# Kernel tuning notes

Measured on AMD Instinct MI355X. Metric: run time of the kernel, lower is better.

The kernel has to match this reference:

```python
import jax, jax.numpy as jnp
import numpy as np

D_MODEL = 1024
D_INNER = 2048  # d_model * expand_factor
EPS = 1e-6


def setup_inputs() -> dict:
    key = jax.random.key(0)
    ks = jax.random.split(key, 9)
    s_in = 1.0 / np.sqrt(D_MODEL)
    s_out = 1.0 / np.sqrt(D_INNER)
    x = jax.random.normal(ks[0], (4, 2048, D_MODEL), dtype=jnp.float32)
    # weights stored as [in, out] (transpose of nn.Linear layout)
    Wq = jax.random.uniform(ks[1], (D_MODEL, D_INNER), jnp.float32, -s_in, s_in)
    bq = jax.random.uniform(ks[2], (D_INNER,), jnp.float32, -s_in, s_in)
    Wk = jax.random.uniform(ks[3], (D_MODEL, D_INNER), jnp.float32, -s_in, s_in)
    bk = jax.random.uniform(ks[4], (D_INNER,), jnp.float32, -s_in, s_in)
    Wv = jax.random.uniform(ks[5], (D_MODEL, D_INNER), jnp.float32, -s_in, s_in)
    bv = jax.random.uniform(ks[6], (D_INNER,), jnp.float32, -s_in, s_in)
    Wo = jax.random.uniform(ks[7], (D_INNER, D_MODEL), jnp.float32, -s_out, s_out)
    bo = jax.random.uniform(ks[8], (D_MODEL,), jnp.float32, -s_out, s_out)
    return {"x": x, "Wq": Wq, "bq": bq, "Wk": Wk, "bk": bk,
            "Wv": Wv, "bv": bv, "Wo": Wo, "bo": bo}


def _phi(x):
    """ELU + 1 feature map (positive features)."""
    return jax.nn.elu(x) + 1.0


def reference(x, Wq, bq, Wk, bk, Wv, bv, Wo, bo):
    # x: [B, N, d_model]
    Q = _phi(x @ Wq + bq)          # [B, N, d_inner]
    K = _phi(x @ Wk + bk)          # [B, N, d_inner]
    V = x @ Wv + bv                # [B, N, d_inner]
    n = x.shape[1]
    # Causal linear attention; identical math to cumsum-of-outer-products:
    # numerator_n = sum_{m<=n} (Q_n . K_m) V_m ; denominator_n = sum_{m<=n} Q_n . K_m
    scores = jnp.einsum("bnd,bmd->bnm", Q, K)            # [B, N, N]
    mask = jnp.tril(jnp.ones((n, n), dtype=scores.dtype))
    scores = scores * mask
    numerator = jnp.einsum("bnm,bme->bne", scores, V)    # [B, N, d_inner]
    denominator = scores.sum(axis=-1, keepdims=True) + EPS
    out = numerator / denominator
    return out @ Wo + bo           # [B, N, d_model] (dropout is identity in eval)
```

## Files before the change

kernel.cpp:

```cpp
#include <hip/hip_runtime.h>
#include <hip/hip_bf16.h>


#define D_MODEL 1024
#define D_INNER 2048
#define SEQ     2048
#define NBATCH  4
#define MTOT    (NBATCH * SEQ)

typedef __attribute__((ext_vector_type(8))) __bf16 bf16x8;
typedef __attribute__((ext_vector_type(4))) float  f32x4;
typedef __attribute__((ext_vector_type(8))) short  short8v;
typedef __attribute__((ext_vector_type(4))) int    int4v;
typedef __attribute__((ext_vector_type(8))) int    int8v;

__device__ __forceinline__ short f2bf(float f) {
  union { float f; unsigned u; } x; x.f = f;
  unsigned r = x.u + 0x7fffu + ((x.u >> 16) & 1u);
  return (short)(r >> 16);
}
__device__ __forceinline__ float bf2f(short s) {
  union { unsigned u; float f; } x; x.u = ((unsigned)(unsigned short)s) << 16;
  return x.f;
}

__device__ __forceinline__ unsigned char f2fp8(float f) {
  union { float f; unsigned u; } x; x.f = f;
  const unsigned s = (x.u >> 24) & 0x80u;
  const unsigned a = x.u & 0x7fffffffu;
  if (a >= 0x43E00000u) return (unsigned char)(s | 0x7Eu);
  if (a < 0x3C800000u) {
    union { float f; unsigned u; } y; y.u = a;
    const int mi = (int)rintf(y.f * 512.0f);
    return (unsigned char)(s | (unsigned)mi);
  }
  const unsigned r = a + 0x7FFFFu + ((a >> 20) & 1u);
  const unsigned E = (r >> 23) - 120u;
  return (unsigned char)(s | (E << 3) | ((r >> 20) & 7u));
}

typedef const void __attribute__((address_space(1)))* as1cv;
typedef void __attribute__((address_space(3)))* as3v;

__device__ __forceinline__ void gload_lds16(const void* g, void* l) {
  __builtin_amdgcn_global_load_lds((as1cv)g, (as3v)l, 16, 0, 0);
}

__device__ __forceinline__ f32x4 mfma16(bf16x8 a, bf16x8 b, f32x4 c) {
  return __builtin_amdgcn_mfma_f32_16x16x32_bf16(a, b, c, 0, 0, 0);
}

__device__ __forceinline__ f32x4 mfma_fp8(int8v a, int8v b, f32x4 c) {
  asm("v_mfma_f32_16x16x128_f8f6f4 %0, %1, %2, %0"
      : "+v"(c) : "v"(a), "v"(b));
  return c;
}

__device__ __forceinline__ void gemm_pipe(const short* __restrict__ A, int lda, int aRowBase,
                                          const short* __restrict__ B, int ldb, int bRowBase,
                                          int k0, int k1, short* smem, f32x4 acc[4][4]) {
  const int t    = threadIdx.x;
  const int lane = t & 63, wid = t >> 6;
  const int wr = wid >> 1, wc = wid & 1;
  const int lrow = lane & 15, kblk = lane >> 4;

  const int r0 = t >> 2;
  const int sc = ((t & 3) ^ ((t >> 3) & 3)) * 8;
  const short* pA = A + (size_t)(aRowBase + r0) * lda + (k0 + sc);
  const short* pB = B + (size_t)(bRowBase + r0) * ldb + (k0 + sc);
  const size_t rA = (size_t)64 * lda;
  const size_t rB = (size_t)64 * ldb;

  int aoff[4], boff[4];
#pragma unroll
  for (int m = 0; m < 4; ++m) {
    const int row = wr * 64 + m * 16 + lrow;
    aoff[m] = (row * 64 + kblk * 16) ^ (((row >> 1) & 3) << 4);
  }
#pragma unroll
  for (int n = 0; n < 4; ++n) {
    const int row = wc * 64 + n * 16 + lrow;
    boff[n] = (row * 64 + kblk * 16) ^ (((row >> 1) & 3) << 4);
  }
  const char* cs = (const char*)smem;

#define STG(bufShorts) do {                                                    \
    gload_lds16(pA, smem + (bufShorts) + t * 8);                               \
    gload_lds16(pA + rA, smem + (bufShorts) + 2048 + t * 8);                   \
    gload_lds16(pB, smem + (bufShorts) + 4096 + t * 8);                        \
    gload_lds16(pB + rB, smem + (bufShorts) + 6144 + t * 8);                   \
    pA += 32; pB += 32;                                                        \
  } while (0)

#define CSTEP(bufBytes) do {                                                   \
    bf16x8 a[4], b[4];                                                         \
    _Pragma("unroll") for (int m = 0; m < 4; ++m)                              \
      a[m] = *(const bf16x8*)(cs + (bufBytes) + aoff[m]);                      \
    _Pragma("unroll") for (int n = 0; n < 4; ++n)                              \
      b[n] = *(const bf16x8*)(cs + (bufBytes) + 8192 + boff[n]);               \
    _Pragma("unroll") for (int m = 0; m < 4; ++m)                              \
      _Pragma("unroll") for (int n = 0; n < 4; ++n)                            \
        acc[m][n] = mfma16(a[m], b[n], acc[m][n]);                             \
  } while (0)

  STG(0);
  __syncthreads();
  for (int k = k0; k < k1; k += 64) {
    if (k + 32 < k1) STG(8192);
    CSTEP(0);
    __syncthreads();
    if (k + 64 < k1) STG(0);
    CSTEP(16384);
    __syncthreads();
  }
#undef STG
#undef CSTEP
}

__device__ __forceinline__ void gemm_pipe8(const unsigned char* __restrict__ A, int lda, int aRowBase,
                                           const unsigned char* __restrict__ B, int ldb, int bRowBase,
                                           int k0, int k1, char* smem, f32x4 acc[4][4]) {
  const int t    = threadIdx.x;
  const int lane = t & 63, wid = t >> 6;
  const int wr = wid >> 1, wc = wid & 1;
  const int lrow = lane & 15, kblk = lane >> 4;

  const int srow = t >> 3;
  const int scol = (((t & 7) ^ ((t >> 3) & 7)) << 4);
  const unsigned char* pA = A + (size_t)(aRowBase + srow) * lda + (k0 + scol);
  const unsigned char* pB = B + (size_t)(bRowBase + srow) * ldb + (k0 + scol);

  int aoff[4][2], boff[4][2];
#pragma unroll
  for (int m = 0; m < 4; ++m) {
    const int row = wr * 64 + m * 16 + lrow;
#pragma unroll
    for (int j = 0; j < 2; ++j)
      aoff[m][j] = row * 128 + (((kblk * 2 + j) ^ (row & 7)) << 4);
  }
#pragma unroll
  for (int n = 0; n < 4; ++n) {
    const int row = wc * 64 + n * 16 + lrow;
#pragma unroll
    for (int j = 0; j < 2; ++j)
      boff[n][j] = row * 128 + (((kblk * 2 + j) ^ (row & 7)) << 4);
  }

#define STG8(bufB) do {                                                        \
    _Pragma("unroll") for (int i = 0; i < 4; ++i) {                            \
      gload_lds16(pA + (size_t)(32 * i) * lda, smem + (bufB) + i * 4096 + t * 16);      \
      gload_lds16(pB + (size_t)(32 * i) * ldb, smem + (bufB) + 16384 + i * 4096 + t * 16); \
    }                                                                          \
    pA += 128; pB += 128;                                                      \
  } while (0)

#define CSTEP8(bufB) do {                                                      \
    int8v a[4], b[4];                                                          \
    _Pragma("unroll") for (int m = 0; m < 4; ++m)                              \
      _Pragma("unroll") for (int j = 0; j < 2; ++j)                            \
        ((int4v*)&a[m])[j] = *(const int4v*)(smem + (bufB) + aoff[m][j]);      \
    _Pragma("unroll") for (int n = 0; n < 4; ++n)                              \
      _Pragma("unroll") for (int j = 0; j < 2; ++j)                            \
        ((int4v*)&b[n])[j] = *(const int4v*)(smem + (bufB) + 16384 + boff[n][j]); \
    _Pragma("unroll") for (int m = 0; m < 4; ++m)                              \
      _Pragma("unroll") for (int n = 0; n < 4; ++n)                            \
        acc[m][n] = mfma_fp8(a[m], b[n], acc[m][n]);                           \
  } while (0)

  STG8(0);
  __syncthreads();
  for (int k = k0; k < k1; k += 256) {
    if (k + 128 < k1) STG8(32768);
    CSTEP8(0);
    __syncthreads();
    if (k + 256 < k1) STG8(0);
    CSTEP8(32768);
    __syncthreads();
  }
#undef STG8
#undef CSTEP8
}

#define GEMM_PRE                                           \
  __shared__ __align__(16) short smem[4 * 4096];           \
  f32x4 acc[4][4];                                         \
  _Pragma("unroll")                                        \
  for (int m = 0; m < 4; ++m)                              \
    _Pragma("unroll")                                      \
    for (int n = 0; n < 4; ++n) acc[m][n] = (f32x4){0.f, 0.f, 0.f, 0.f};

#define GEMM_PRE8                                          \
  __shared__ __align__(16) char smem8[65536];              \
  f32x4 acc[4][4];                                         \
  _Pragma("unroll")                                        \
  for (int m = 0; m < 4; ++m)                              \
    _Pragma("unroll")                                      \
    for (int n = 0; n < 4; ++n) acc[m][n] = (f32x4){0.f, 0.f, 0.f, 0.f};

#define EPILOG_VARS                                        \
  const int lane = threadIdx.x & 63;                       \
  const int wid  = threadIdx.x >> 6;                       \
  const int wr = wid >> 1, wc = wid & 1;                   \
  const int lrow = lane & 15, kblk = lane >> 4;

__device__ __forceinline__ void retile_store(const short* smem, short* dst0, int ldd) {
  const int er  = threadIdx.x >> 1;
  const int hf  = threadIdx.x & 1;
  short* dst = dst0 + (size_t)er * ldd + hf * 64;
#pragma unroll
  for (int i = 0; i < 8; ++i) {
    int byte = er * 256 + hf * 128 + i * 16;
    byte ^= (er & 7) << 5;
    ((short8v*)dst)[i] = *(const short8v*)((const char*)smem + byte);
  }
}

__global__ __launch_bounds__(256) void k_proj_qk8(const unsigned char* __restrict__ X8,
                                                  const unsigned char* __restrict__ WT8,
                                                  const float* __restrict__ bq,
                                                  const float* __restrict__ bk,
                                                  unsigned char* __restrict__ Qm8,
                                                  unsigned char* __restrict__ Km8) {
  GEMM_PRE8
  const int blockM = blockIdx.y * 128;
  const int blockN = blockIdx.x * 128;
  gemm_pipe8(X8, D_MODEL, blockM, WT8, D_MODEL, blockN, 0, D_MODEL, smem8, acc);
  EPILOG_VARS
  const int seg = blockN >> 11;
  const float* bias = (seg == 0) ? bq : bk;
  unsigned char* dst = (seg == 0) ? Qm8 : Km8;
#pragma unroll
  for (int m = 0; m < 4; ++m)
#pragma unroll
    for (int n = 0; n < 4; ++n) {
      const int e = (blockN & 2047) + wc * 64 + n * 16 + lrow;
      const float bvv = bias[e];
#pragma unroll
      for (int j = 0; j < 4; ++j) {
        const int row = blockM + wr * 64 + m * 16 + kblk * 4 + j;
        float v = acc[m][n][j] + bvv;
        v = (v > 0.f) ? (v + 1.f) : __expf(v);
        dst[(size_t)row * D_INNER + e] = f2fp8(v);
      }
    }
}

__global__ __launch_bounds__(256) void k_wfuse(const short* __restrict__ WvB,
                                               const short* __restrict__ WoT,
                                               short* __restrict__ wfT) {
  GEMM_PRE
  const int blockM = blockIdx.y * 128;
  const int blockN = blockIdx.x * 128;
  gemm_pipe(WvB, D_INNER, blockM, WoT, D_INNER, blockN, 0, D_INNER, smem, acc);
  EPILOG_VARS
#pragma unroll
  for (int m = 0; m < 4; ++m)
#pragma unroll
    for (int n = 0; n < 4; ++n) {
      const int cl = wc * 64 + n * 16 + lrow;
#pragma unroll
      for (int j = 0; j < 4; ++j) {
        const int rl = wr * 64 + m * 16 + kblk * 4 + j;
        int byte = cl * 256 + rl * 2;
        byte ^= (cl & 7) << 5;
        *(short*)((char*)smem + byte) = f2bf(acc[m][n][j]);
      }
    }
  __syncthreads();
  retile_store(smem, wfT + (size_t)blockN * D_MODEL + blockM, D_MODEL);
}

__global__ __launch_bounds__(256) void k_bfuse(const float* __restrict__ bv,
                                               const float* __restrict__ Wo,
                                               float* __restrict__ bfuse) {
  const int o = blockIdx.x;
  const int t = threadIdx.x;
  float s = 0.f;
#pragma unroll
  for (int e = t; e < D_INNER; e += 256)
    s += bv[e] * Wo[(size_t)e * D_MODEL + o];
#pragma unroll
  for (int off = 32; off >= 1; off >>= 1) s += __shfl_down(s, off, 64);
  __shared__ float ws[4];
  if ((t & 63) == 0) ws[t >> 6] = s;
  __syncthreads();
  if (t == 0) bfuse[o] = ws[0] + ws[1] + ws[2] + ws[3];
}

__global__ __launch_bounds__(256) void k_w2(const short* __restrict__ X,
                                            const short* __restrict__ WfT,
                                            const float* __restrict__ bfuse,
                                            short* __restrict__ w2T) {
  GEMM_PRE
  const int blockM = blockIdx.y * 128;
  const int blockN = blockIdx.x * 128;
  gemm_pipe(X, D_MODEL, blockM, WfT, D_MODEL, blockN, 0, D_MODEL, smem, acc);
  EPILOG_VARS
#pragma unroll
  for (int m = 0; m < 4; ++m)
#pragma unroll
    for (int n = 0; n < 4; ++n) {
      const int cl = wc * 64 + n * 16 + lrow;
      const float bvv = bfuse[blockN + cl];
#pragma unroll
      for (int j = 0; j < 4; ++j) {
        const int rl = wr * 64 + m * 16 + kblk * 4 + j;
        int byte = cl * 256 + rl * 2;
        byte ^= (cl & 7) << 5;
        *(short*)((char*)smem + byte) = f2bf(acc[m][n][j] + bvv);
      }
    }
  __syncthreads();
  const int b   = blockM >> 11;
  const int mm0 = blockM & 2047;
  retile_store(smem, w2T + ((size_t)b * D_MODEL + blockN) * SEQ + mm0, SEQ);
}

__global__ __launch_bounds__(256) void k_qkt8(const unsigned char* __restrict__ Q8,
                                              const unsigned char* __restrict__ K8,
                                              short* __restrict__ S,
                                              float* __restrict__ den_part) {
  const int b = blockIdx.y;
  const int t = blockIdx.x;
  int ib = (int)((-1.0f + sqrtf(8.0f * (float)t + 1.0f)) * 0.5f);
  while ((ib + 1) * (ib + 2) / 2 <= t) ++ib;
  while (ib * (ib + 1) / 2 > t) --ib;
  const int jb = t - ib * (ib + 1) / 2;
  GEMM_PRE8
  short* Sb = S + (size_t)b * SEQ * SEQ;
  gemm_pipe8(Q8 + (size_t)b * SEQ * D_INNER, D_INNER, ib * 128,
             K8 + (size_t)b * SEQ * D_INNER, D_INNER, jb * 128,
             0, D_INNER, smem8, acc);
  EPILOG_VARS
  const bool diag = (jb == ib);
  float sums[4][4];
#pragma unroll
  for (int m = 0; m < 4; ++m)
#pragma unroll
    for (int j = 0; j < 4; ++j) sums[m][j] = 0.f;
#pragma unroll
  for (int m = 0; m < 4; ++m)
#pragma unroll
    for (int n = 0; n < 4; ++n) {
      const int col = jb * 128 + wc * 64 + n * 16 + lrow;
#pragma unroll
      for (int j = 0; j < 4; ++j) {
        const int row = ib * 128 + wr * 64 + m * 16 + kblk * 4 + j;
        float v = acc[m][n][j];
        if (diag && col > row) v = 0.f;
        const short bs = f2bf(v);
        Sb[(size_t)row * SEQ + col] = bs;
        sums[m][j] += bf2f(bs);
      }
    }
#pragma unroll
  for (int m = 0; m < 4; ++m)
#pragma unroll
    for (int j = 0; j < 4; ++j) {
      float red = sums[m][j];
      red += __shfl_xor(red, 1, 64);
      red += __shfl_xor(red, 2, 64);
      red += __shfl_xor(red, 4, 64);
      red += __shfl_xor(red, 8, 64);
      if (lrow == 0) {
        const int rloc = wr * 64 + m * 16 + kblk * 4 + j;
        den_part[(size_t)(2 * jb + wc) * MTOT + b * SEQ + ib * 128 + rloc] = red;
      }
    }
}

__global__ __launch_bounds__(256) void k_sv(const short* __restrict__ S,
                                            const short* __restrict__ W2T,
                                            const float* __restrict__ den_part,
                                            const float* __restrict__ bo,
                                            float* __restrict__ out) {
  const int b = blockIdx.z;
  const int ib = 15 - blockIdx.y;
  const int eb = blockIdx.x;
  __shared__ float dnm[128];
  {
    const int t = threadIdx.x;
    if (t < 128) {
      float s = 1e-6f;
      const int nv = 2 * (ib + 1);
      const float* dp = den_part + b * SEQ + ib * 128 + t;
      for (int q = 0; q < nv; ++q) s += dp[(size_t)q * MTOT];
      dnm[t] = 1.0f / s;
    }
  }
  GEMM_PRE
  gemm_pipe(S + (size_t)b * SEQ * SEQ, SEQ, ib * 128,
            W2T + (size_t)b * (size_t)D_MODEL * SEQ, SEQ, eb * 128,
            0, (ib + 1) * 128, smem, acc);
  EPILOG_VARS
  const int blockM = ib * 128;
#pragma unroll
  for (int m = 0; m < 4; ++m)
#pragma unroll
    for (int j = 0; j < 4; ++j) {
      const int rloc = wr * 64 + m * 16 + kblk * 4 + j;
      const int row = blockM + rloc;
      const float rcp = dnm[rloc];
#pragma unroll
      for (int n = 0; n < 4; ++n) {
        const int col = eb * 128 + wc * 64 + n * 16 + lrow;
        out[((size_t)(b * SEQ + row)) * D_MODEL + col] = acc[m][n][j] * rcp + bo[col];
      }
    }
}

__global__ void k_cvt(const float* __restrict__ in, short* __restrict__ outb,
                      unsigned char* __restrict__ out8, int n4) {
  int i = blockIdx.x * blockDim.x + threadIdx.x;
  const int stride = gridDim.x * blockDim.x;
  for (; i < n4; i += stride) {
    float4 v = ((const float4*)in)[i];
    short4 o;
    o.x = f2bf(v.x); o.y = f2bf(v.y); o.z = f2bf(v.z); o.w = f2bf(v.w);
    ((short4*)outb)[i] = o;
    uchar4 q;
    q.x = f2fp8(v.x); q.y = f2fp8(v.y); q.z = f2fp8(v.z); q.w = f2fp8(v.w);
    ((uchar4*)out8)[i] = q;
  }
}

__global__ __launch_bounds__(256) void k_transposeAll(const float* __restrict__ w0,
                                                      const float* __restrict__ w1,
                                                      const float* __restrict__ w2,
                                                      const float* __restrict__ w3,
                                                      unsigned char* __restrict__ wqkT8,
                                                      short* __restrict__ wvB,
                                                      short* __restrict__ woT) {
  __shared__ float tl[32][33];
  const int z = blockIdx.z;
  const float* in = (z == 0) ? w0 : (z == 1) ? w1 : (z == 2) ? w2 : w3;
  const int R = (z < 3) ? 1024 : 2048;
  const int C = (z < 3) ? 2048 : 1024;
  const int nbx = C >> 5;
  const int c0 = (blockIdx.x % nbx) * 32, r0 = (blockIdx.x / nbx) * 32;
  const int tx = threadIdx.x & 31, ty = (threadIdx.x >> 5) * 4;
  if (z == 2) {
#pragma unroll
    for (int i = 0; i < 4; ++i) {
      const size_t idx = (size_t)(r0 + ty + i) * C + (c0 + tx);
      wvB[idx] = f2bf(in[idx]);
    }
    return;
  }
#pragma unroll
  for (int i = 0; i < 4; ++i)
    tl[ty + i][tx] = in[(size_t)(r0 + ty + i) * C + (c0 + tx)];
  __syncthreads();
  if (z < 2) {
    unsigned char* o = wqkT8 + (size_t)z * D_INNER * D_MODEL;
#pragma unroll
    for (int i = 0; i < 4; ++i)
      o[(size_t)(c0 + ty + i) * R + (r0 + tx)] = f2fp8(tl[tx][ty + i]);
  } else {
#pragma unroll
    for (int i = 0; i < 4; ++i)
      woT[(size_t)(c0 + ty + i) * R + (r0 + tx)] = f2bf(tl[tx][ty + i]);
  }
}

extern "C" void kernel_launch(void* const* d_in, const int* in_sizes, int n_in,
                              void* d_out, int out_size, void* d_ws, size_t ws_size,
                              hipStream_t stream) {
  const float* x  = (const float*)d_in[0];
  const float* Wq = (const float*)d_in[1];
  const float* bq = (const float*)d_in[2];
  const float* Wk = (const float*)d_in[3];
  const float* bk = (const float*)d_in[4];
  const float* Wv = (const float*)d_in[5];
  const float* bv = (const float*)d_in[6];
  const float* Wo = (const float*)d_in[7];
  const float* bo = (const float*)d_in[8];
  float* out = (float*)d_out;

  short* xb    = (short*)d_ws;
  short* wvB   = xb    + (size_t)MTOT * D_MODEL;
  short* woT   = wvB   + (size_t)D_MODEL * D_INNER;
  short* wfT   = woT   + (size_t)D_MODEL * D_INNER;
  short* Sc    = wfT   + (size_t)D_MODEL * D_MODEL;
  short* w2T   = Sc    + (size_t)NBATCH * SEQ * SEQ;
  unsigned char* x8    = (unsigned char*)(w2T + (size_t)NBATCH * D_MODEL * SEQ);
  unsigned char* wqkT8 = x8    + (size_t)MTOT * D_MODEL;
  unsigned char* Qm8   = wqkT8 + (size_t)2 * D_INNER * D_MODEL;
  unsigned char* Km8   = Qm8   + (size_t)MTOT * D_INNER;
  float* den_part      = (float*)(Km8 + (size_t)MTOT * D_INNER);
  float* bfuse         = den_part + (size_t)32 * MTOT;

  dim3 b256(256);
  k_cvt<<<2048, b256, 0, stream>>>(x, xb, x8, MTOT * D_MODEL / 4);
  k_transposeAll<<<dim3(2048, 1, 4), b256, 0, stream>>>(Wq, Wk, Wv, Wo, wqkT8, wvB, woT);

  k_bfuse<<<1024, b256, 0, stream>>>(bv, Wo, bfuse);
  k_wfuse<<<dim3(8, 8), b256, 0, stream>>>(wvB, woT, wfT);

  k_proj_qk8<<<dim3(32, 64), b256, 0, stream>>>(x8, wqkT8, bq, bk, Qm8, Km8);
  k_qkt8<<<dim3(136, NBATCH), b256, 0, stream>>>(Qm8, Km8, Sc, den_part);

  k_w2<<<dim3(8, 64), b256, 0, stream>>>(xb, wfT, bfuse, w2T);
  k_sv<<<dim3(8, 16, NBATCH), b256, 0, stream>>>(Sc, w2T, den_part, bo, out);
}
```

Baseline: 263.6 us.

## Merge preprocessing kernels and use single-buffered fp8 QK^T pipeline

Three preprocessing kernels (x conversion, weight transpose/cast, fused bias) are combined into one launch that dispatches by block index, removing two kernel launches and their gaps. Separately, the QK^T fp8 GEMM switches to a single-buffered 32KB LDS loop with one K-step of 128 per iteration. The smaller LDS footprint may allow more blocks per CU, but it gives up overlapping loads with MFMA compute. In the merged kernel, a block that returns early in the Wv path is harmless, since that path has no barrier after the return.

Result: no change. 262.4 us (median of 2 runs) (-0.4%).

```diff
diff --git a/kernel.cpp b/kernel.cpp
--- a/kernel.cpp
+++ b/kernel.cpp
@@ -181,6 +181,63 @@
 #undef CSTEP8
 }
 
+__device__ __forceinline__ void gemm_pipe8s(const unsigned char* __restrict__ A, int lda, int aRowBase,
+                                            const unsigned char* __restrict__ B, int ldb, int bRowBase,
+                                            int k0, int k1, char* smem, f32x4 acc[4][4]) {
+  const int t    = threadIdx.x;
+  const int lane = t & 63, wid = t >> 6;
+  const int wr = wid >> 1, wc = wid & 1;
+  const int lrow = lane & 15, kblk = lane >> 4;
+
+  const int srow = t >> 3;
+  const int scol = (((t & 7) ^ ((t >> 3) & 7)) << 4);
+  const unsigned char* pA = A + (size_t)(aRowBase + srow) * lda + (k0 + scol);
+  const unsigned char* pB = B + (size_t)(bRowBase + srow) * ldb + (k0 + scol);
+
+  int aoff[4][2], boff[4][2];
+#pragma unroll
+  for (int m = 0; m < 4; ++m) {
+    const int row = wr * 64 + m * 16 + lrow;
+#pragma unroll
+    for (int j = 0; j < 2; ++j)
+      aoff[m][j] = row * 128 + (((kblk * 2 + j) ^ (row & 7)) << 4);
+  }
+#pragma unroll
+  for (int n = 0; n < 4; ++n) {
+    const int row = wc * 64 + n * 16 + lrow;
+#pragma unroll
+    for (int j = 0; j < 2; ++j)
+      boff[n][j] = row * 128 + (((kblk * 2 + j) ^ (row & 7)) << 4);
+  }
+
+  for (int k = k0; k < k1; k += 128) {
+#pragma unroll
+    for (int i = 0; i < 4; ++i) {
+      gload_lds16(pA + (size_t)(32 * i) * lda, smem + i * 4096 + t * 16);
+      gload_lds16(pB + (size_t)(32 * i) * ldb, smem + 16384 + i * 4096 + t * 16);
+    }
+    pA += 128; pB += 128;
+    __syncthreads();
+    int8v a[4], b[4];
+#pragma unroll
+    for (int m = 0; m < 4; ++m)
+#pragma unroll
+      for (int j = 0; j < 2; ++j)
+        ((int4v*)&a[m])[j] = *(const int4v*)(smem + aoff[m][j]);
+#pragma unroll
+    for (int n = 0; n < 4; ++n)
+#pragma unroll
+      for (int j = 0; j < 2; ++j)
+        ((int4v*)&b[n])[j] = *(const int4v*)(smem + 16384 + boff[n][j]);
+#pragma unroll
+    for (int m = 0; m < 4; ++m)
+#pragma unroll
+      for (int n = 0; n < 4; ++n)
+        acc[m][n] = mfma_fp8(a[m], b[n], acc[m][n]);
+    __syncthreads();
+  }
+}
+
 #define GEMM_PRE                                           \
   __shared__ __align__(16) short smem[4 * 4096];           \
   f32x4 acc[4][4];                                         \
@@ -191,6 +248,14 @@
 
 #define GEMM_PRE8                                          \
   __shared__ __align__(16) char smem8[65536];              \
+  f32x4 acc[4][4];                                         \
+  _Pragma("unroll")                                        \
+  for (int m = 0; m < 4; ++m)                              \
+    _Pragma("unroll")                                      \
+    for (int n = 0; n < 4; ++n) acc[m][n] = (f32x4){0.f, 0.f, 0.f, 0.f};
+
+#define GEMM_PRE8S                                         \
+  __shared__ __align__(16) char smem8[32768];              \
   f32x4 acc[4][4];                                         \
   _Pragma("unroll")                                        \
   for (int m = 0; m < 4; ++m)                              \
@@ -270,23 +335,6 @@
   retile_store(smem, wfT + (size_t)blockN * D_MODEL + blockM, D_MODEL);
 }
 
-__global__ __launch_bounds__(256) void k_bfuse(const float* __restrict__ bv,
-                                               const float* __restrict__ Wo,
-                                               float* __restrict__ bfuse) {
-  const int o = blockIdx.x;
-  const int t = threadIdx.x;
-  float s = 0.f;
-#pragma unroll
-  for (int e = t; e < D_INNER; e += 256)
-    s += bv[e] * Wo[(size_t)e * D_MODEL + o];
-#pragma unroll
-  for (int off = 32; off >= 1; off >>= 1) s += __shfl_down(s, off, 64);
-  __shared__ float ws[4];
-  if ((t & 63) == 0) ws[t >> 6] = s;
-  __syncthreads();
-  if (t == 0) bfuse[o] = ws[0] + ws[1] + ws[2] + ws[3];
-}
-
 __global__ __launch_bounds__(256) void k_w2(const short* __restrict__ X,
                                             const short* __restrict__ WfT,
                                             const float* __restrict__ bfuse,
@@ -326,11 +374,11 @@
   while ((ib + 1) * (ib + 2) / 2 <= t) ++ib;
   while (ib * (ib + 1) / 2 > t) --ib;
   const int jb = t - ib * (ib + 1) / 2;
-  GEMM_PRE8
+  GEMM_PRE8S
   short* Sb = S + (size_t)b * SEQ * SEQ;
-  gemm_pipe8(Q8 + (size_t)b * SEQ * D_INNER, D_INNER, ib * 128,
-             K8 + (size_t)b * SEQ * D_INNER, D_INNER, jb * 128,
-             0, D_INNER, smem8, acc);
+  gemm_pipe8s(Q8 + (size_t)b * SEQ * D_INNER, D_INNER, ib * 128,
+              K8 + (size_t)b * SEQ * D_INNER, D_INNER, jb * 128,
+              0, D_INNER, smem8, acc);
   EPILOG_VARS
   const bool diag = (jb == ib);
   float sums[4][4];
@@ -409,57 +457,77 @@
     }
 }
 
-__global__ void k_cvt(const float* __restrict__ in, short* __restrict__ outb,
-                      unsigned char* __restrict__ out8, int n4) {
-  int i = blockIdx.x * blockDim.x + threadIdx.x;
-  const int stride = gridDim.x * blockDim.x;
-  for (; i < n4; i += stride) {
-    float4 v = ((const float4*)in)[i];
-    short4 o;
-    o.x = f2bf(v.x); o.y = f2bf(v.y); o.z = f2bf(v.z); o.w = f2bf(v.w);
-    ((short4*)outb)[i] = o;
-    uchar4 q;
-    q.x = f2fp8(v.x); q.y = f2fp8(v.y); q.z = f2fp8(v.z); q.w = f2fp8(v.w);
-    ((uchar4*)out8)[i] = q;
-  }
-}
-
-__global__ __launch_bounds__(256) void k_transposeAll(const float* __restrict__ w0,
-                                                      const float* __restrict__ w1,
-                                                      const float* __restrict__ w2,
-                                                      const float* __restrict__ w3,
-                                                      unsigned char* __restrict__ wqkT8,
-                                                      short* __restrict__ wvB,
-                                                      short* __restrict__ woT) {
+__global__ __launch_bounds__(256) void k_pre(const float* __restrict__ x,
+                                             const float* __restrict__ Wq,
+                                             const float* __restrict__ Wk,
+                                             const float* __restrict__ Wv,
+                                             const float* __restrict__ Wo,
+                                             const float* __restrict__ bv,
+                                             short* __restrict__ xb,
+                                             unsigned char* __restrict__ x8,
+                                             unsigned char* __restrict__ wqkT8,
+                                             short* __restrict__ wvB,
+                                             short* __restrict__ woT,
+                                             float* __restrict__ bfuse) {
   __shared__ float tl[32][33];
-  const int z = blockIdx.z;
-  const float* in = (z == 0) ? w0 : (z == 1) ? w1 : (z == 2) ? w2 : w3;
-  const int R = (z < 3) ? 1024 : 2048;
-  const int C = (z < 3) ? 2048 : 1024;
-  const int nbx = C >> 5;
-  const int c0 = (blockIdx.x % nbx) * 32, r0 = (blockIdx.x / nbx) * 32;
-  const int tx = threadIdx.x & 31, ty = (threadIdx.x >> 5) * 4;
-  if (z == 2) {
-#pragma unroll
-    for (int i = 0; i < 4; ++i) {
-      const size_t idx = (size_t)(r0 + ty + i) * C + (c0 + tx);
-      wvB[idx] = f2bf(in[idx]);
-    }
-    return;
-  }
-#pragma unroll
-  for (int i = 0; i < 4; ++i)
-    tl[ty + i][tx] = in[(size_t)(r0 + ty + i) * C + (c0 + tx)];
-  __syncthreads();
-  if (z < 2) {
-    unsigned char* o = wqkT8 + (size_t)z * D_INNER * D_MODEL;
+  __shared__ float ws[4];
+  const int bid = blockIdx.x;
+  if (bid < 2048) {
+    const int n4 = MTOT * D_MODEL / 4;
+    int i = bid * 256 + threadIdx.x;
+    const int stride = 2048 * 256;
+    for (; i < n4; i += stride) {
+      float4 v = ((const float4*)x)[i];
+      short4 o;
+      o.x = f2bf(v.x); o.y = f2bf(v.y); o.z = f2bf(v.z); o.w = f2bf(v.w);
+      ((short4*)xb)[i] = o;
+      uchar4 q;
+      q.x = f2fp8(v.x); q.y = f2fp8(v.y); q.z = f2fp8(v.z); q.w = f2fp8(v.w);
+      ((uchar4*)x8)[i] = q;
+    }
+  } else if (bid < 2048 + 4 * 2048) {
+    const int z  = (bid - 2048) >> 11;
+    const int bx = (bid - 2048) & 2047;
+    const float* in = (z == 0) ? Wq : (z == 1) ? Wk : (z == 2) ? Wv : Wo;
+    const int R = (z < 3) ? 1024 : 2048;
+    const int C = (z < 3) ? 2048 : 1024;
+    const int nbx = C >> 5;
+    const int c0 = (bx % nbx) * 32, r0 = (bx / nbx) * 32;
+    const int tx = threadIdx.x & 31, ty = (threadIdx.x >> 5) * 4;
+    if (z == 2) {
+#pragma unroll
+      for (int i = 0; i < 4; ++i) {
+        const size_t idx = (size_t)(r0 + ty + i) * C + (c0 + tx);
+        wvB[idx] = f2bf(in[idx]);
+      }
+      return;
+    }
 #pragma unroll
     for (int i = 0; i < 4; ++i)
-      o[(size_t)(c0 + ty + i) * R + (r0 + tx)] = f2fp8(tl[tx][ty + i]);
+      tl[ty + i][tx] = in[(size_t)(r0 + ty + i) * C + (c0 + tx)];
+    __syncthreads();
+    if (z < 2) {
+      unsigned char* o = wqkT8 + (size_t)z * D_INNER * D_MODEL;
+#pragma unroll
+      for (int i = 0; i < 4; ++i)
+        o[(size_t)(c0 + ty + i) * R + (r0 + tx)] = f2fp8(tl[tx][ty + i]);
+    } else {
+#pragma unroll
+      for (int i = 0; i < 4; ++i)
+        woT[(size_t)(c0 + ty + i) * R + (r0 + tx)] = f2bf(tl[tx][ty + i]);
+    }
   } else {
-#pragma unroll
-    for (int i = 0; i < 4; ++i)
-      woT[(size_t)(c0 + ty + i) * R + (r0 + tx)] = f2bf(tl[tx][ty + i]);
+    const int o = bid - (2048 + 4 * 2048);
+    const int t = threadIdx.x;
+    float s = 0.f;
+#pragma unroll
+    for (int e = t; e < D_INNER; e += 256)
+      s += bv[e] * Wo[(size_t)e * D_MODEL + o];
+#pragma unroll
+    for (int off = 32; off >= 1; off >>= 1) s += __shfl_down(s, off, 64);
+    if ((t & 63) == 0) ws[t >> 6] = s;
+    __syncthreads();
+    if (t == 0) bfuse[o] = ws[0] + ws[1] + ws[2] + ws[3];
   }
 }
 
@@ -491,10 +559,8 @@
   float* bfuse         = den_part + (size_t)32 * MTOT;
 
   dim3 b256(256);
-  k_cvt<<<2048, b256, 0, stream>>>(x, xb, x8, MTOT * D_MODEL / 4);
-  k_transposeAll<<<dim3(2048, 1, 4), b256, 0, stream>>>(Wq, Wk, Wv, Wo, wqkT8, wvB, woT);
-
-  k_bfuse<<<1024, b256, 0, stream>>>(bv, Wo, bfuse);
+  k_pre<<<11264, b256, 0, stream>>>(x, Wq, Wk, Wv, Wo, bv,
+                                    xb, x8, wqkT8, wvB, woT, bfuse);
   k_wfuse<<<dim3(8, 8), b256, 0, stream>>>(wvB, woT, wfT);
 
   k_proj_qk8<<<dim3(32, 64), b256, 0, stream>>>(x8, wqkT8, bq, bk, Qm8, Km8);
```
